# Performance work log

Measured on AMD Instinct MI355X. Metric: run time of the kernel, lower is better.

## Reference

```python
import jax, jax.numpy as jnp
import numpy as np

EMBED = 768
HEADS = 12
FFN = 3072
EPS = 1e-5

def _linear_params(key, din, dout):
    k1, k2 = jax.random.split(key)
    s = 1.0 / np.sqrt(din)
    W = jax.random.uniform(k1, (din, dout), minval=-s, maxval=s, dtype=jnp.float32)
    b = jax.random.uniform(k2, (dout,), minval=-s, maxval=s, dtype=jnp.float32)
    return W, b

def setup_inputs() -> dict:
    key = jax.random.key(0)
    ks = jax.random.split(key, 8)
    x = jax.random.normal(ks[0], (1, 4096, EMBED), dtype=jnp.float32)
    Wq, bq = _linear_params(ks[1], EMBED, EMBED)
    Wk, bk = _linear_params(ks[2], EMBED, EMBED)
    Wv, bv = _linear_params(ks[3], EMBED, EMBED)
    Wo, bo = _linear_params(ks[4], EMBED, EMBED)
    W1, b1 = _linear_params(ks[5], EMBED, FFN)
    W2, b2 = _linear_params(ks[6], FFN, EMBED)
    ln1_g = jnp.ones((EMBED,), jnp.float32); ln1_b = jnp.zeros((EMBED,), jnp.float32)
    ln2_g = jnp.ones((EMBED,), jnp.float32); ln2_b = jnp.zeros((EMBED,), jnp.float32)
    return {"x": x, "Wq": Wq, "bq": bq, "Wk": Wk, "bk": bk, "Wv": Wv, "bv": bv,
            "Wo": Wo, "bo": bo, "ln1_g": ln1_g, "ln1_b": ln1_b,
            "ln2_g": ln2_g, "ln2_b": ln2_b, "W1": W1, "b1": b1, "W2": W2, "b2": b2}

def _layernorm(x, g, b):
    mu = jnp.mean(x, axis=-1, keepdims=True)
    var = jnp.mean(jnp.square(x - mu), axis=-1, keepdims=True)
    return (x - mu) * jax.lax.rsqrt(var + EPS) * g + b

def _block(x, Wq, bq, Wk, bk, Wv, bv, Wo, bo, ln1_g, ln1_b, ln2_g, ln2_b, W1, b1, W2, b2):
    B, T, C = x.shape
    H = HEADS
    D = C // H
    # pre-LN
    h = _layernorm(x, ln1_g, ln1_b)
    # naive causal self-attention with explicit [B,H,T,T] scores (as in source)
    q = (h @ Wq + bq).reshape(B, T, H, D).transpose(0, 2, 1, 3)  # bhtd
    k = (h @ Wk + bk).reshape(B, T, H, D).transpose(0, 2, 1, 3)
    v = (h @ Wv + bv).reshape(B, T, H, D).transpose(0, 2, 1, 3)
    scores = jnp.einsum('bhqd,bhkd->bhqk', q, k) / jnp.sqrt(jnp.float32(D))
    causal = jnp.tril(jnp.ones((T, T), dtype=bool))  # True = keep
    scores = jnp.where(causal, scores, -jnp.inf)
    attn = jax.nn.softmax(scores, axis=-1)
    ctx = jnp.einsum('bhqk,bhkd->bhqd', attn, v)
    ctx = ctx.transpose(0, 2, 1, 3).reshape(B, T, C)
    y = ctx @ Wo + bo
    x = y + h  # residual onto ln1 output (source adds to post-LN x)
    # second LN + MLP
    h2 = _layernorm(x, ln2_g, ln2_b)
    m = jax.nn.gelu(h2 @ W1 + b1, approximate=False) @ W2 + b2
    return m + h2

def reference(x, Wq, bq, Wk, bk, Wv, bv, Wo, bo, ln1_g, ln1_b, ln2_g, ln2_b, W1, b1, W2, b2):
    return _block(x, Wq, bq, Wk, bk, Wv, bv, Wo, bo, ln1_g, ln1_b, ln2_g, ln2_b, W1, b1, W2, b2)
```

## Files before the change

### kernel.cpp

```cpp
#include <hip/hip_runtime.h>
#include <math.h>

#define EMBED 768
#define FFN_D 3072
#define TSEQ 4096
#define NHEAD 12
#define DHEAD 64
#define CQKV 2304
#define NSPLIT 4
#define NQITEMS 192
#define SC2Q 0.180336880111120419f

typedef _Float16 f16;
typedef __attribute__((ext_vector_type(2))) _Float16 f16x2;
typedef __attribute__((ext_vector_type(4))) _Float16 f16x4;
typedef __attribute__((ext_vector_type(8))) _Float16 f16x8;
typedef __attribute__((ext_vector_type(4))) float f32x4;

#if __has_builtin(__builtin_amdgcn_exp2f)
#define EXP2(x) __builtin_amdgcn_exp2f(x)
#else
#define EXP2(x) exp2f(x)
#endif

__device__ __forceinline__ f16x2 pkrtz(float a, float b) {
    return __builtin_bit_cast(f16x2, __builtin_amdgcn_cvt_pkrtz(a, b));
}

__device__ __forceinline__ void gload16(const f16* g, f16* lds) {
    __builtin_amdgcn_global_load_lds((const __attribute__((address_space(1))) void*)g,
                                     (__attribute__((address_space(3))) void*)lds, 16, 0, 0);
}

__global__ __launch_bounds__(256) void prep_kernel(const float* __restrict__ Wq,
                                                   const float* __restrict__ Wk,
                                                   const float* __restrict__ Wv,
                                                   const float* __restrict__ Wo,
                                                   const float* __restrict__ W1,
                                                   const float* __restrict__ W2,
                                                   const float* __restrict__ bq,
                                                   const float* __restrict__ bk,
                                                   const float* __restrict__ bv,
                                                   f16* __restrict__ WqkvT,
                                                   f16* __restrict__ WoT,
                                                   f16* __restrict__ W1T,
                                                   f16* __restrict__ W2T,
                                                   float* __restrict__ bqkv) {
    const int b = blockIdx.x;
    const int t = threadIdx.x;
    if (b == 1728) {
#pragma unroll
        for (int i = 0; i < 9; i++) {
            int idx = i * 256 + t;
            if (idx < 768) bqkv[idx] = bq[idx];
            else if (idx < 1536) bqkv[idx] = bk[idx - 768];
            else if (idx < 2304) bqkv[idx] = bv[idx - 1536];
        }
        return;
    }
    const float* W; f16* WT; int din, dout, local;
    if (b < 144)       { W = Wq; WT = WqkvT;                 din = 768;  dout = 768;  local = b; }
    else if (b < 288)  { W = Wk; WT = WqkvT + 768 * 768;     din = 768;  dout = 768;  local = b - 144; }
    else if (b < 432)  { W = Wv; WT = WqkvT + 2 * 768 * 768; din = 768;  dout = 768;  local = b - 288; }
    else if (b < 576)  { W = Wo; WT = WoT;                   din = 768;  dout = 768;  local = b - 432; }
    else if (b < 1152) { W = W1; WT = W1T;                   din = 768;  dout = 3072; local = b - 576; }
    else               { W = W2; WT = W2T;                   din = 3072; dout = 768;  local = b - 1152; }
    const int ntx = dout / 64;
    const int j0 = (local % ntx) * 64;
    const int i0 = (local / ntx) * 64;
    __shared__ float tile[64][65];
    const int tx = t & 63;
    const int ty = t >> 6;
#pragma unroll
    for (int rr = ty; rr < 64; rr += 4)
        tile[rr][tx] = W[(size_t)(i0 + rr) * dout + j0 + tx];
    __syncthreads();
    const int half = t & 31;
    const int rw = t >> 5;
#pragma unroll
    for (int rr = rw; rr < 64; rr += 8) {
        f16x2 v = {(f16)tile[2 * half][rr], (f16)tile[2 * half + 1][rr]};
        *(f16x2*)&WT[(size_t)(j0 + rr) * din + i0 + 2 * half] = v;
    }
}

__global__ __launch_bounds__(256) void ln_kernel(const float* __restrict__ x,
                                                 const float* __restrict__ g,
                                                 const float* __restrict__ b,
                                                 f16* __restrict__ hh) {
    const int row = blockIdx.x;
    const float* xr = x + (size_t)row * EMBED;
    const int t = threadIdx.x;
    float v0 = xr[t], v1 = xr[t + 256], v2 = xr[t + 512];
    float s = v0 + v1 + v2;
#pragma unroll
    for (int m = 1; m < 64; m <<= 1) s += __shfl_xor(s, m);
    __shared__ float red[4], red2[4];
    const int wid = t >> 6, lane = t & 63;
    if (lane == 0) red[wid] = s;
    __syncthreads();
    float mean = (red[0] + red[1] + red[2] + red[3]) * (1.0f / 768.0f);
    float d0 = v0 - mean, d1 = v1 - mean, d2 = v2 - mean;
    float ss = d0 * d0 + d1 * d1 + d2 * d2;
#pragma unroll
    for (int m = 1; m < 64; m <<= 1) ss += __shfl_xor(ss, m);
    if (lane == 0) red2[wid] = ss;
    __syncthreads();
    float inv = rsqrtf((red2[0] + red2[1] + red2[2] + red2[3]) * (1.0f / 768.0f) + 1e-5f);
    size_t base = (size_t)row * EMBED;
    hh[base + t]       = (f16)(d0 * inv * g[t] + b[t]);
    hh[base + t + 256] = (f16)(d1 * inv * g[t + 256] + b[t + 256]);
    hh[base + t + 512] = (f16)(d2 * inv * g[t + 512] + b[t + 512]);
}

template <int EPI, int BM, int BN, int KSTEP>
__global__ __launch_bounds__(256) void gemm_kernel(const f16* __restrict__ A,
                                                   const f16* __restrict__ BT,
                                                   const float* __restrict__ bias,
                                                   const f16* __restrict__ resh,
                                                   float* __restrict__ outf,
                                                   f16* __restrict__ outh,
                                                   f16* __restrict__ vtout,
                                                   int M, int N, int K) {
    constexpr int IM = BM / 32;
    constexpr int JN = BN / 32;
    __shared__ __align__(16) f16 As[KSTEP][BM][64];
    __shared__ __align__(16) f16 Bs[KSTEP][BN][64];
    const int t = threadIdx.x;
    const int nbx = gridDim.x;
    const int nwg = nbx * gridDim.y;
    int bid = blockIdx.x + blockIdx.y * nbx;
    bid = (bid & 7) * (nwg >> 3) + (bid >> 3);
    const int m0 = (bid / nbx) * BM;
    const int n0 = (bid % nbx) * BN;
    const int wid = t >> 6;
    const int lane = t & 63;
    const int wm = (wid >> 1) * (BM / 2);
    const int wn = (wid & 1) * (BN / 2);
    const int lr = lane & 15;
    const int quad = lane >> 4;
    const int sr = lane >> 3;
    const int scn = (lane & 7) ^ sr;
    const int xv = lr & 7;

    f32x4 zero = {0.f, 0.f, 0.f, 0.f};
    f32x4 acc[IM][JN];
#pragma unroll
    for (int i = 0; i < IM; i++)
#pragma unroll
        for (int j = 0; j < JN; j++) acc[i][j] = zero;

    const f16* Ap = A + (size_t)(m0 + wid * (BM / 4) + sr) * K + scn * 8;
    const f16* Bp = BT + (size_t)(n0 + wid * (BN / 4) + sr) * K + scn * 8;

    for (int k0 = 0; k0 < K; k0 += 64 * KSTEP) {
        __syncthreads();
#pragma unroll
        for (int sub = 0; sub < KSTEP; sub++) {
#pragma unroll
            for (int c = 0; c < BM / 32; c++)
                gload16(Ap + (size_t)(c * 8) * K + k0 + sub * 64, &As[sub][wid * (BM / 4) + c * 8][0]);
#pragma unroll
            for (int c = 0; c < BN / 32; c++)
                gload16(Bp + (size_t)(c * 8) * K + k0 + sub * 64, &Bs[sub][wid * (BN / 4) + c * 8][0]);
        }
        __syncthreads();
#pragma unroll
        for (int sub = 0; sub < KSTEP; sub++) {
#pragma unroll
            for (int ks = 0; ks < 2; ks++) {
                f16x8 af[IM], bf[JN];
#pragma unroll
                for (int i = 0; i < IM; i++)
                    af[i] = *(const f16x8*)&As[sub][wm + i * 16 + lr][((ks * 4 + quad) ^ xv) * 8];
#pragma unroll
                for (int j = 0; j < JN; j++)
                    bf[j] = *(const f16x8*)&Bs[sub][wn + j * 16 + lr][((ks * 4 + quad) ^ xv) * 8];
#pragma unroll
                for (int i = 0; i < IM; i++)
#pragma unroll
                    for (int j = 0; j < JN; j++)
                        acc[i][j] = __builtin_amdgcn_mfma_f32_16x16x32_f16(bf[j], af[i], acc[i][j], 0, 0, 0);
            }
        }
    }

    const bool vsec = (EPI == 0) && (n0 >= 2 * EMBED);
#pragma unroll
    for (int i = 0; i < IM; i++) {
        const int row = m0 + wm + i * 16 + lr;
#pragma unroll
        for (int j = 0; j < JN; j++) {
            const int col = n0 + wn + j * 16 + quad * 4;
            const float4 bv = *(const float4*)&bias[col];
            float v0 = acc[i][j][0] + bv.x;
            float v1 = acc[i][j][1] + bv.y;
            float v2 = acc[i][j][2] + bv.z;
            float v3 = acc[i][j][3] + bv.w;
            const size_t idx = (size_t)row * N + col;
            if (EPI == 0) {
                if (vsec) {
                    const int c0 = col - 2 * EMBED;
                    vtout[(size_t)(c0 + 0) * TSEQ + row] = (f16)v0;
                    vtout[(size_t)(c0 + 1) * TSEQ + row] = (f16)v1;
                    vtout[(size_t)(c0 + 2) * TSEQ + row] = (f16)v2;
                    vtout[(size_t)(c0 + 3) * TSEQ + row] = (f16)v3;
                } else {
                    const float qs = (col < EMBED) ? SC2Q : 1.0f;
                    f16x4 hv = {(f16)(v0 * qs), (f16)(v1 * qs), (f16)(v2 * qs), (f16)(v3 * qs)};
                    *(f16x4*)&outh[idx] = hv;
                }
            } else if (EPI == 1) {
                const f16x4 rr = *(const f16x4*)&resh[idx];
                f32x4 ov = {v0 + (float)rr[0], v1 + (float)rr[1], v2 + (float)rr[2], v3 + (float)rr[3]};
                *(f32x4*)&outf[idx] = ov;
            } else {
                f16x4 hv = {(f16)(0.5f * v0 * (1.0f + erff(v0 * 0.70710678118654752f))),
                            (f16)(0.5f * v1 * (1.0f + erff(v1 * 0.70710678118654752f))),
                            (f16)(0.5f * v2 * (1.0f + erff(v2 * 0.70710678118654752f))),
                            (f16)(0.5f * v3 * (1.0f + erff(v3 * 0.70710678118654752f)))};
                *(f16x4*)&outh[idx] = hv;
            }
        }
    }
}

__global__ __launch_bounds__(256) void attn_kernel(const f16* __restrict__ qkv,
                                                   const f16* __restrict__ vT,
                                                   f16* __restrict__ OpartH,
                                                   float2* __restrict__ ml,
                                                   int* __restrict__ ctr) {
    __shared__ __align__(16) f16 Ks[64][72];
    __shared__ __align__(16) f16 Vt[64][72];
    __shared__ int s_item;
    const int t = threadIdx.x;
    const int wid = t >> 6;
    const int lane = t & 63;
    const int lr = lane & 15;
    const int quad = lane >> 4;
    const int srow = t >> 3;
    const int scol = (t & 7) * 8;
    const int pA = (t & 1) * 16 + ((t >> 1) & 1) * 4 + (t & 4) * 8;
    const int xq = blockIdx.x & 7;

    for (;;) {
        __syncthreads();
        if (t == 0) s_item = atomicAdd(&ctr[xq], 1);
        __syncthreads();
        const int item = s_item;
        if (item >= NQITEMS) return;
        const int qb = 31 - item / 6;
        const int u = xq * 6 + item % 6;
        const int h = u >> 2;
        const int sp = u & 3;
        const int q0 = qb * 128;

        const int nkb = 2 * qb + 2;
        const int chunk = (nkb + NSPLIT - 1) / NSPLIT;
        const int kb0 = sp * chunk;
        const int kb1 = min(nkb, kb0 + chunk);
        const int wrow0 = q0 + wid * 32;

        float m_i[2] = {-INFINITY, -INFINITY};
        float l_lane[2] = {0.f, 0.f};
        f32x4 zero = {0.f, 0.f, 0.f, 0.f};
        f32x4 o[4][2];
#pragma unroll
        for (int dt = 0; dt < 4; dt++)
#pragma unroll
            for (int qt = 0; qt < 2; qt++) o[dt][qt] = zero;

        f16x8 qf[2][2];
        int4 kreg[2], vreg[2];
        const f16* kbase = qkv + EMBED + (size_t)h * DHEAD;
        const f16* vbase = vT + (size_t)h * DHEAD * TSEQ;
        if (kb0 < kb1) {
#pragma unroll
            for (int qt = 0; qt < 2; qt++)
#pragma unroll
                for (int dh = 0; dh < 2; dh++)
                    qf[qt][dh] = *(const f16x8*)(qkv + (size_t)(wrow0 + qt * 16 + lr) * CQKV
                                                 + h * DHEAD + dh * 32 + quad * 8);
            const int k0 = kb0 * 64;
#pragma unroll
            for (int p = 0; p < 2; p++) {
                kreg[p] = *(const int4*)(kbase + (size_t)(k0 + p * 32 + srow) * CQKV + scol);
                vreg[p] = *(const int4*)(vbase + (size_t)(p * 32 + srow) * TSEQ + k0 + scol);
            }
        }

        for (int kb = kb0; kb < kb1; ++kb) {
            const int k0 = kb * 64;
            __syncthreads();
#pragma unroll
            for (int p = 0; p < 2; p++) {
                *(int4*)&Ks[p * 32 + srow][scol] = kreg[p];
                *(int2*)&Vt[p * 32 + srow][pA]     = make_int2(vreg[p].x, vreg[p].y);
                *(int2*)&Vt[p * 32 + srow][pA + 8] = make_int2(vreg[p].z, vreg[p].w);
            }
            __syncthreads();
            if (kb + 1 < kb1) {
                const int kn = (kb + 1) * 64;
#pragma unroll
                for (int p = 0; p < 2; p++) {
                    kreg[p] = *(const int4*)(kbase + (size_t)(kn + p * 32 + srow) * CQKV + scol);
                    vreg[p] = *(const int4*)(vbase + (size_t)(p * 32 + srow) * TSEQ + kn + scol);
                }
            }

            if (k0 <= wrow0 + 31) {
                f32x4 s[4][2];
#pragma unroll
                for (int kt = 0; kt < 4; kt++)
#pragma unroll
                    for (int qt = 0; qt < 2; qt++) s[kt][qt] = zero;
#pragma unroll
                for (int dh = 0; dh < 2; dh++) {
#pragma unroll
                    for (int kt = 0; kt < 4; kt++) {
                        f16x8 kf = *(const f16x8*)&Ks[kt * 16 + lr][dh * 32 + quad * 8];
#pragma unroll
                        for (int qt = 0; qt < 2; qt++)
                            s[kt][qt] = __builtin_amdgcn_mfma_f32_16x16x32_f16(kf, qf[qt][dh], s[kt][qt], 0, 0, 0);
                    }
                }
                if (k0 + 63 > wrow0) {
#pragma unroll
                    for (int kt = 0; kt < 4; kt++)
#pragma unroll
                        for (int qt = 0; qt < 2; qt++)
#pragma unroll
                            for (int r = 0; r < 4; r++) {
                                int key = k0 + kt * 16 + quad * 4 + r;
                                int row = wrow0 + qt * 16 + lr;
                                if (key > row) s[kt][qt][r] = -INFINITY;
                            }
                }
                float mx[2];
#pragma unroll
                for (int qt = 0; qt < 2; qt++) {
                    float a[4];
#pragma unroll
                    for (int kt = 0; kt < 4; kt++)
                        a[kt] = fmaxf(fmaxf(s[kt][qt][0], s[kt][qt][1]),
                                      fmaxf(s[kt][qt][2], s[kt][qt][3]));
                    float m = fmaxf(fmaxf(a[0], a[1]), fmaxf(a[2], a[3]));
                    m = fmaxf(m, __shfl_xor(m, 16));
                    m = fmaxf(m, __shfl_xor(m, 32));
                    mx[qt] = m;
                }
                if (__any((mx[0] > m_i[0] + 4.f) || (mx[1] > m_i[1] + 4.f))) {
#pragma unroll
                    for (int qt = 0; qt < 2; qt++) {
                        float mn = fmaxf(m_i[qt], mx[qt]);
                        float al = EXP2(m_i[qt] - mn);
                        m_i[qt] = mn;
                        l_lane[qt] *= al;
#pragma unroll
                        for (int dt = 0; dt < 4; dt++)
#pragma unroll
                            for (int r = 0; r < 4; r++) o[dt][qt][r] *= al;
                    }
                }
                union PW { f16x8 v8; f16x2 h2[4]; };
                PW pw[2][2];
                float rs[2] = {0.f, 0.f};
#pragma unroll
                for (int kt = 0; kt < 4; kt++)
#pragma unroll
                    for (int qt = 0; qt < 2; qt++) {
                        float p0 = EXP2(s[kt][qt][0] - m_i[qt]);
                        float p1 = EXP2(s[kt][qt][1] - m_i[qt]);
                        float p2 = EXP2(s[kt][qt][2] - m_i[qt]);
                        float p3 = EXP2(s[kt][qt][3] - m_i[qt]);
                        rs[qt] += (p0 + p1) + (p2 + p3);
                        pw[kt >> 1][qt].h2[(kt & 1) * 2]     = pkrtz(p0, p1);
                        pw[kt >> 1][qt].h2[(kt & 1) * 2 + 1] = pkrtz(p2, p3);
                    }
#pragma unroll
                for (int qt = 0; qt < 2; qt++) l_lane[qt] += rs[qt];
#pragma unroll
                for (int s2 = 0; s2 < 2; s2++)
#pragma unroll
                    for (int dt = 0; dt < 4; dt++) {
                        f16x8 vf = *(const f16x8*)&Vt[dt * 16 + lr][s2 * 32 + quad * 8];
#pragma unroll
                        for (int qt = 0; qt < 2; qt++)
                            o[dt][qt] = __builtin_amdgcn_mfma_f32_16x16x32_f16(vf, pw[s2][qt].v8, o[dt][qt], 0, 0, 0);
                    }
            }
        }

        float l_i[2];
#pragma unroll
        for (int qt = 0; qt < 2; qt++) {
            float v2 = l_lane[qt];
            v2 += __shfl_xor(v2, 16);
            v2 += __shfl_xor(v2, 32);
            l_i[qt] = v2;
        }
        __syncthreads();
        f16* ob = ((wid & 2) ? &Vt[0][0] : &Ks[0][0]) + (wid & 1) * (32 * 72);
#pragma unroll
        for (int qt = 0; qt < 2; qt++)
#pragma unroll
            for (int dt = 0; dt < 4; dt++) {
                f16x4 oh = {(f16)o[dt][qt][0], (f16)o[dt][qt][1], (f16)o[dt][qt][2], (f16)o[dt][qt][3]};
                *(f16x4*)&ob[(qt * 16 + lr) * 72 + dt * 16 + quad * 4] = oh;
            }
        const int rl = lane >> 3;
        const int ck = lane & 7;
#pragma unroll
        for (int i = 0; i < 4; i++) {
            const int row_l = rl + i * 8;
            f16x8 val = *(const f16x8*)&ob[row_l * 72 + ck * 8];
            *(f16x8*)&OpartH[((size_t)sp * TSEQ + wrow0 + row_l) * EMBED + h * DHEAD + ck * 8] = val;
        }
#pragma unroll
        for (int qt = 0; qt < 2; qt++)
            if (quad == 0) {
                int row = wrow0 + qt * 16 + lr;
                ml[((size_t)sp * TSEQ + row) * NHEAD + h] = make_float2(m_i[qt], l_i[qt]);
            }
    }
}

__global__ __launch_bounds__(128) void attn_merge_kernel(const f16* __restrict__ OpartH,
                                                         const float2* __restrict__ ml,
                                                         f16* __restrict__ ctx) {
    const int row = blockIdx.x;
    const int t = threadIdx.x;
    __shared__ float wgt[NSPLIT][NHEAD];
    if (t < NHEAD) {
        float m[NSPLIT], l[NSPLIT];
        float M = -INFINITY;
#pragma unroll
        for (int s = 0; s < NSPLIT; s++) {
            float2 v = ml[((size_t)s * TSEQ + row) * NHEAD + t];
            m[s] = v.x; l[s] = v.y;
            M = fmaxf(M, m[s]);
        }
        float L = 0.f;
        float w[NSPLIT];
#pragma unroll
        for (int s = 0; s < NSPLIT; s++) {
            w[s] = exp2f(m[s] - M);
            L += l[s] * w[s];
        }
        float rL = 1.0f / L;
#pragma unroll
        for (int s = 0; s < NSPLIT; s++) wgt[s][t] = w[s] * rL;
    }
    __syncthreads();
    if (t < 96) {
        const int h = t >> 3;
        float acc[8] = {0.f, 0.f, 0.f, 0.f, 0.f, 0.f, 0.f, 0.f};
#pragma unroll
        for (int s = 0; s < NSPLIT; s++) {
            const float w = wgt[s][h];
            f16x8 v = *(const f16x8*)&OpartH[((size_t)s * TSEQ + row) * EMBED + t * 8];
#pragma unroll
            for (int e = 0; e < 8; e++) acc[e] += w * (float)v[e];
        }
        f16x8 out;
#pragma unroll
        for (int e = 0; e < 8; e++) out[e] = (f16)acc[e];
        *(f16x8*)&ctx[(size_t)row * EMBED + t * 8] = out;
    }
}

extern "C" void kernel_launch(void* const* d_in, const int* in_sizes, int n_in,
                              void* d_out, int out_size, void* d_ws, size_t ws_size,
                              hipStream_t stream) {
    const float* x     = (const float*)d_in[0];
    const float* Wq    = (const float*)d_in[1];
    const float* bq    = (const float*)d_in[2];
    const float* Wk    = (const float*)d_in[3];
    const float* bk    = (const float*)d_in[4];
    const float* Wv    = (const float*)d_in[5];
    const float* bv    = (const float*)d_in[6];
    const float* Wo    = (const float*)d_in[7];
    const float* bo    = (const float*)d_in[8];
    const float* ln1_g = (const float*)d_in[9];
    const float* ln1_b = (const float*)d_in[10];
    const float* ln2_g = (const float*)d_in[11];
    const float* ln2_b = (const float*)d_in[12];
    const float* W1    = (const float*)d_in[13];
    const float* b1    = (const float*)d_in[14];
    const float* W2    = (const float*)d_in[15];
    const float* b2    = (const float*)d_in[16];

    char* p = (char*)d_ws;
    auto alloc = [&](size_t bytes) -> void* {
        void* r = (void*)p;
        p += (bytes + 255) & ~(size_t)255;
        return r;
    };
    f16*   WqkvT = (f16*)alloc((size_t)CQKV * EMBED * 2);
    f16*   WoT   = (f16*)alloc((size_t)EMBED * EMBED * 2);
    f16*   W1T   = (f16*)alloc((size_t)FFN_D * EMBED * 2);
    f16*   W2T   = (f16*)alloc((size_t)EMBED * FFN_D * 2);
    float* bqkv  = (float*)alloc((size_t)CQKV * 4);
    f16*   hh    = (f16*)alloc((size_t)TSEQ * EMBED * 2);
    f16*   qkv   = (f16*)alloc((size_t)TSEQ * CQKV * 2);
    f16*   vT    = (f16*)alloc((size_t)EMBED * TSEQ * 2);
    f16*   ctx   = (f16*)alloc((size_t)TSEQ * EMBED * 2);
    float* x2    = (float*)alloc((size_t)TSEQ * EMBED * 4);
    f16*   h2h   = (f16*)alloc((size_t)TSEQ * EMBED * 2);
    f16*   m1    = (f16*)alloc((size_t)TSEQ * FFN_D * 2);
    int*   ctr   = (int*)alloc(256);

    f16*    OpartH = m1;
    float2* mlbuf  = (float2*)x2;

    dim3 blk(256);
    prep_kernel<<<dim3(1729), blk, 0, stream>>>(Wq, Wk, Wv, Wo, W1, W2, bq, bk, bv,
                                                WqkvT, WoT, W1T, W2T, bqkv);
    ln_kernel<<<dim3(TSEQ), blk, 0, stream>>>(x, ln1_g, ln1_b, hh);
    gemm_kernel<0, 64, 128, 2><<<dim3(CQKV / 128, TSEQ / 64), blk, 0, stream>>>(
        hh, WqkvT, bqkv, nullptr, nullptr, qkv, vT, TSEQ, CQKV, EMBED);
    (void)hipMemsetAsync(ctr, 0, 256, stream);
    attn_kernel<<<dim3(768), blk, 0, stream>>>(qkv, vT, OpartH, mlbuf, ctr);
    attn_merge_kernel<<<dim3(TSEQ), dim3(128), 0, stream>>>(OpartH, mlbuf, ctx);
    gemm_kernel<1, 64, 64, 2><<<dim3(EMBED / 64, TSEQ / 64), blk, 0, stream>>>(
        ctx, WoT, bo, hh, x2, nullptr, nullptr, TSEQ, EMBED, EMBED);
    ln_kernel<<<dim3(TSEQ), blk, 0, stream>>>(x2, ln2_g, ln2_b, h2h);
    gemm_kernel<2, 128, 128, 1><<<dim3(FFN_D / 128, TSEQ / 128), blk, 0, stream>>>(
        h2h, W1T, b1, nullptr, nullptr, m1, nullptr, TSEQ, FFN_D, EMBED);
    gemm_kernel<1, 64, 64, 2><<<dim3(EMBED / 64, TSEQ / 64), blk, 0, stream>>>(
        m1, W2T, b2, h2h, (float*)d_out, nullptr, nullptr, TSEQ, EMBED, FFN_D);
}
```

Before: 308.9 us.

## Prefetch GEMM tiles through registers with padded LDS instead of direct global-to-LDS loads

Replaces the direct global_load_lds staging in the GEMM with register prefetch. The next K-tile is loaded into registers while MFMA runs on the current LDS tile, then stored to LDS. The XOR swizzle is replaced by row padding (72 halves) to avoid bank conflicts, and the QKV GEMM drops to KSTEP=1. The aim is to overlap global latency with compute, at the cost of more VGPRs, extra LDS store instructions and larger shared memory.

Measured after the change: 619.8 us. 101% more time.

```diff
diff --git a/kernel.cpp b/kernel.cpp
--- a/kernel.cpp
+++ b/kernel.cpp
@@ -25,11 +25,6 @@
 
 __device__ __forceinline__ f16x2 pkrtz(float a, float b) {
     return __builtin_bit_cast(f16x2, __builtin_amdgcn_cvt_pkrtz(a, b));
-}
-
-__device__ __forceinline__ void gload16(const f16* g, f16* lds) {
-    __builtin_amdgcn_global_load_lds((const __attribute__((address_space(1))) void*)g,
-                                     (__attribute__((address_space(3))) void*)lds, 16, 0, 0);
 }
 
 __global__ __launch_bounds__(256) void prep_kernel(const float* __restrict__ Wq,
@@ -124,8 +119,10 @@
                                                    int M, int N, int K) {
     constexpr int IM = BM / 32;
     constexpr int JN = BN / 32;
-    __shared__ __align__(16) f16 As[KSTEP][BM][64];
-    __shared__ __align__(16) f16 Bs[KSTEP][BN][64];
+    constexpr int AC = BM / 32;
+    constexpr int BC = BN / 32;
+    __shared__ __align__(16) f16 As[KSTEP][BM][72];
+    __shared__ __align__(16) f16 Bs[KSTEP][BN][72];
     const int t = threadIdx.x;
     const int nbx = gridDim.x;
     const int nwg = nbx * gridDim.y;
@@ -140,8 +137,7 @@
     const int lr = lane & 15;
     const int quad = lane >> 4;
     const int sr = lane >> 3;
-    const int scn = (lane & 7) ^ sr;
-    const int xv = lr & 7;
+    const int ccol = (lane & 7) * 8;
 
     f32x4 zero = {0.f, 0.f, 0.f, 0.f};
     f32x4 acc[IM][JN];
@@ -150,21 +146,46 @@
 #pragma unroll
         for (int j = 0; j < JN; j++) acc[i][j] = zero;
 
-    const f16* Ap = A + (size_t)(m0 + wid * (BM / 4) + sr) * K + scn * 8;
-    const f16* Bp = BT + (size_t)(n0 + wid * (BN / 4) + sr) * K + scn * 8;
+    const f16* Ap = A + (size_t)(m0 + wid * (BM / 4) + sr) * K + ccol;
+    const f16* Bp = BT + (size_t)(n0 + wid * (BN / 4) + sr) * K + ccol;
+    const int arow = wid * (BM / 4) + sr;
+    const int brow = wid * (BN / 4) + sr;
+
+    int4 areg[KSTEP][AC], breg[KSTEP][BC];
+#pragma unroll
+    for (int sub = 0; sub < KSTEP; sub++) {
+#pragma unroll
+        for (int c = 0; c < AC; c++)
+            areg[sub][c] = *(const int4*)(Ap + (size_t)(c * 8) * K + sub * 64);
+#pragma unroll
+        for (int c = 0; c < BC; c++)
+            breg[sub][c] = *(const int4*)(Bp + (size_t)(c * 8) * K + sub * 64);
+    }
 
     for (int k0 = 0; k0 < K; k0 += 64 * KSTEP) {
         __syncthreads();
 #pragma unroll
         for (int sub = 0; sub < KSTEP; sub++) {
 #pragma unroll
-            for (int c = 0; c < BM / 32; c++)
-                gload16(Ap + (size_t)(c * 8) * K + k0 + sub * 64, &As[sub][wid * (BM / 4) + c * 8][0]);
-#pragma unroll
-            for (int c = 0; c < BN / 32; c++)
-                gload16(Bp + (size_t)(c * 8) * K + k0 + sub * 64, &Bs[sub][wid * (BN / 4) + c * 8][0]);
+            for (int c = 0; c < AC; c++)
+                *(int4*)&As[sub][arow + c * 8][ccol] = areg[sub][c];
+#pragma unroll
+            for (int c = 0; c < BC; c++)
+                *(int4*)&Bs[sub][brow + c * 8][ccol] = breg[sub][c];
         }
         __syncthreads();
+        if (k0 + 64 * KSTEP < K) {
+            const int kn = k0 + 64 * KSTEP;
+#pragma unroll
+            for (int sub = 0; sub < KSTEP; sub++) {
+#pragma unroll
+                for (int c = 0; c < AC; c++)
+                    areg[sub][c] = *(const int4*)(Ap + (size_t)(c * 8) * K + kn + sub * 64);
+#pragma unroll
+                for (int c = 0; c < BC; c++)
+                    breg[sub][c] = *(const int4*)(Bp + (size_t)(c * 8) * K + kn + sub * 64);
+            }
+        }
 #pragma unroll
         for (int sub = 0; sub < KSTEP; sub++) {
 #pragma unroll
@@ -172,10 +193,10 @@
                 f16x8 af[IM], bf[JN];
 #pragma unroll
                 for (int i = 0; i < IM; i++)
-                    af[i] = *(const f16x8*)&As[sub][wm + i * 16 + lr][((ks * 4 + quad) ^ xv) * 8];
+                    af[i] = *(const f16x8*)&As[sub][wm + i * 16 + lr][(ks * 4 + quad) * 8];
 #pragma unroll
                 for (int j = 0; j < JN; j++)
-                    bf[j] = *(const f16x8*)&Bs[sub][wn + j * 16 + lr][((ks * 4 + quad) ^ xv) * 8];
+                    bf[j] = *(const f16x8*)&Bs[sub][wn + j * 16 + lr][(ks * 4 + quad) * 8];
 #pragma unroll
                 for (int i = 0; i < IM; i++)
 #pragma unroll
@@ -517,7 +538,7 @@
     prep_kernel<<<dim3(1729), blk, 0, stream>>>(Wq, Wk, Wv, Wo, W1, W2, bq, bk, bv,
                                                 WqkvT, WoT, W1T, W2T, bqkv);
     ln_kernel<<<dim3(TSEQ), blk, 0, stream>>>(x, ln1_g, ln1_b, hh);
-    gemm_kernel<0, 64, 128, 2><<<dim3(CQKV / 128, TSEQ / 64), blk, 0, stream>>>(
+    gemm_kernel<0, 64, 128, 1><<<dim3(CQKV / 128, TSEQ / 64), blk, 0, stream>>>(
         hh, WqkvT, bqkv, nullptr, nullptr, qkv, vT, TSEQ, CQKV, EMBED);
     (void)hipMemsetAsync(ctr, 0, 256, stream);
     attn_kernel<<<dim3(768), blk, 0, stream>>>(qkv, vT, OpartH, mlbuf, ctr);
```
